# Performance work log

Hardware: AMD Instinct MI355X
Metric: run time of the kernel (lower is better)

Reference implementation:

```python
import jax, jax.numpy as jnp
import numpy as np

B, N, C = 4, 2048, 768
H = 12
D = C // H  # head_dim = 64
SCALE = D ** -0.5


def setup_inputs() -> dict:
    key = jax.random.key(0)
    ks = jax.random.split(key, 9)
    x_q = jax.random.normal(ks[0], (B, N, C), dtype=jnp.float32)
    x_k = jax.random.normal(ks[1], (B, N, C), dtype=jnp.float32)
    x_v = jax.random.normal(ks[2], (B, N, C), dtype=jnp.float32)
    x_u = jax.random.uniform(ks[3], (B, N, C), dtype=jnp.float32)
    s = C ** -0.5
    Wq = jax.random.normal(ks[4], (C, C), dtype=jnp.float32) * s
    Wk = jax.random.normal(ks[5], (C, C), dtype=jnp.float32) * s
    Wv = jax.random.normal(ks[6], (C, C), dtype=jnp.float32) * s
    Wp = jax.random.normal(ks[7], (C, C), dtype=jnp.float32) * s
    bp = jax.random.normal(ks[8], (C,), dtype=jnp.float32) * 0.01
    return {"x_q": x_q, "x_k": x_k, "x_v": x_v, "x_u": x_u,
            "Wq": Wq, "Wk": Wk, "Wv": Wv, "Wp": Wp, "bp": bp}


def reference(x_q, x_k, x_v, x_u, Wq, Wk, Wv, Wp, bp):
    # Linear projections (torch Linear: y = x @ W.T), split into heads [B,H,N,D]
    def to_heads(x, W):
        y = jnp.einsum('bnc,oc->bno', x, W)
        return y.reshape(B, N, H, D).transpose(0, 2, 1, 3)
    q = to_heads(x_q, Wq) * SCALE
    k = to_heads(x_k, Wk)
    v = to_heads(x_v, Wv)
    # Scores [B,H,N,N]
    attn = jnp.einsum('bhqd,bhkd->bhqk', q, k)
    # Uncertainty map: per-query scalar (mean over channels), broadcast over keys & heads
    uc = jnp.mean(x_u, axis=-1)  # [B,N]
    attn = attn * uc[:, None, :, None]
    attn = jax.nn.softmax(attn, axis=-1)
    out = jnp.einsum('bhqk,bhkd->bhqd', attn, v)
    out = out.transpose(0, 2, 1, 3).reshape(B, N, C)
    return jnp.einsum('bnc,oc->bno', out, Wp) + bp
```

## Files before the change

### kernel.cpp

```cpp
#include <hip/hip_runtime.h>
#include <hip/hip_bf16.h>
#include <cstdint>

#define B_ 4
#define N_ 2048
#define C_ 768
#define H_ 12
#define D_ 64
#define QSCALE 0.18033688011112042f

typedef __bf16 bf16x8 __attribute__((ext_vector_type(8)));
typedef float f32x4 __attribute__((ext_vector_type(4)));
typedef float f32x16 __attribute__((ext_vector_type(16)));

__device__ __forceinline__ unsigned f2bs(float x) {
  unsigned u = __builtin_bit_cast(unsigned, x);
  unsigned r = (u + 0x7fffu + ((u >> 16) & 1u)) >> 16;
  return r;
}

__device__ __forceinline__ bf16x8 ldb8(const unsigned short* p) {
  return __builtin_bit_cast(bf16x8, *(const uint4*)p);
}

__device__ __forceinline__ f32x4 mfma16(bf16x8 a, bf16x8 b, f32x4 c) {
  return __builtin_amdgcn_mfma_f32_16x16x32_bf16(a, b, c, 0, 0, 0);
}

__device__ __forceinline__ f32x16 mfma32(bf16x8 a, bf16x8 b, f32x16 c) {
  return __builtin_amdgcn_mfma_f32_32x32x16_bf16(a, b, c, 0, 0, 0);
}

__device__ __forceinline__ void async16(const unsigned short* g, unsigned short* l) {
  __builtin_amdgcn_global_load_lds(
      (const __attribute__((address_space(1))) unsigned int*)g,
      (__attribute__((address_space(3))) unsigned int*)l, 16, 0, 0);
}

__global__ void prep_kernel(
    const float* __restrict__ xq, const float* __restrict__ xk,
    const float* __restrict__ xv, const float* __restrict__ xu,
    const float* __restrict__ Wq, const float* __restrict__ Wk,
    const float* __restrict__ Wv, const float* __restrict__ Wp,
    unsigned short* __restrict__ dxq, unsigned short* __restrict__ dxk,
    unsigned short* __restrict__ dxv,
    unsigned short* __restrict__ dwq, unsigned short* __restrict__ dwk,
    unsigned short* __restrict__ dwv, unsigned short* __restrict__ dwp,
    float* __restrict__ uc) {
  const int id = blockIdx.x;
  if (id < 5184) {
    const float* s;
    unsigned short* d;
    int sub;
    if (id < 4608) {
      s = (id < 1536) ? xq : (id < 3072) ? xk : xv;
      d = (id < 1536) ? dxq : (id < 3072) ? dxk : dxv;
      sub = (id < 1536) ? id : (id < 3072) ? (id - 1536) : (id - 3072);
    } else {
      int t = id - 4608;
      int which = t / 144;
      s = (which == 0) ? Wq : (which == 1) ? Wk : (which == 2) ? Wv : Wp;
      d = (which == 0) ? dwq : (which == 1) ? dwk : (which == 2) ? dwv : dwp;
      sub = t % 144;
    }
    const int base = sub * 4096 + (int)threadIdx.x * 4;
#pragma unroll
    for (int st = 0; st < 4; ++st) {
      int i = base + st * 1024;
      float4 v = *(const float4*)(s + i);
      ushort4 h;
      h.x = (unsigned short)f2bs(v.x); h.y = (unsigned short)f2bs(v.y);
      h.z = (unsigned short)f2bs(v.z); h.w = (unsigned short)f2bs(v.w);
      *(ushort4*)(d + i) = h;
    }
  } else {
    int sub = id - 5184;
    int w = threadIdx.x >> 6, lane = threadIdx.x & 63;
    int row = sub * 4 + w;
    const float* p = xu + (size_t)row * C_;
    float s = 0.f;
#pragma unroll
    for (int i = 0; i < 3; ++i) {
      float4 v = *(const float4*)(p + (i * 64 + lane) * 4);
      s += v.x + v.y + v.z + v.w;
    }
#pragma unroll
    for (int off = 1; off < 64; off <<= 1) s += __shfl_xor(s, off);
    if (lane == 0) uc[row] = s * (1.f / 768.f);
  }
}

#define TSTR 136
__global__ __launch_bounds__(256, 3) void gemm_qkv(
    const unsigned short* __restrict__ xq, const unsigned short* __restrict__ xk,
    const unsigned short* __restrict__ xv,
    const unsigned short* __restrict__ wq, const unsigned short* __restrict__ wk,
    const unsigned short* __restrict__ wv,
    unsigned short* __restrict__ oq, unsigned short* __restrict__ ok,
    unsigned short* __restrict__ ov, const float* __restrict__ uc) {
  __shared__ __align__(16) unsigned short S[192 * TSTR];
  unsigned short* Al = S;
  unsigned short* Bl = S + 8192;
  const int tid = threadIdx.x;
  const int w = tid >> 6, lane = tid & 63, quad = lane >> 4, id15 = lane & 15;
  const int wm = (w >> 1) << 6, wn = (w & 1) * 96;
  const int id = blockIdx.x;
  const int xcd = id & 7, slot = id >> 3;
  const int n0 = (slot & 3) * 192;
  const int gz = xcd * 24 + (slot >> 2);
  const int z = gz >> 6, m0 = (gz & 63) << 7;

  const unsigned short* A = (z == 0) ? xq : (z == 1) ? xk : xv;
  const unsigned short* W = (z == 0) ? wq : (z == 1) ? wk : wv;

  const int wb = tid & 192;
  const unsigned short* ap[4];
#pragma unroll
  for (int s = 0; s < 4; ++s) {
    int g = s * 256 + tid;
    int row = (g >> 2) & 127;
    int col = ((g >> 9) << 5) | ((g & 3) << 3);
    ap[s] = A + (size_t)(m0 + row) * C_ + col;
  }
  const unsigned short* bp[6];
#pragma unroll
  for (int s = 0; s < 6; ++s) {
    int g = s * 256 + tid;
    int r4 = g >> 2;
    int pan = (g >= 768) ? 1 : 0;
    int row = r4 - pan * 192;
    int col = pan * 32 + ((g & 3) << 3);
    bp[s] = W + (size_t)(n0 + row) * C_ + col;
  }

  f32x4 acc[4][6] = {};
  for (int kt = 0; kt < C_; kt += 64) {
    __syncthreads();
#pragma unroll
    for (int s = 0; s < 4; ++s) async16(ap[s] + kt, Al + (s * 256 + wb) * 8);
#pragma unroll
    for (int s = 0; s < 6; ++s) async16(bp[s] + kt, Bl + (s * 256 + wb) * 8);
    __syncthreads();

#pragma unroll
    for (int kk = 0; kk < 2; ++kk) {
      bf16x8 af[4], bfr[6];
#pragma unroll
      for (int i = 0; i < 4; ++i)
        af[i]  = ldb8(&Al[kk * 4096 + (wm + i * 16 + id15) * 32 + quad * 8]);
#pragma unroll
      for (int j = 0; j < 6; ++j)
        bfr[j] = ldb8(&Bl[kk * 6144 + (wn + j * 16 + id15) * 32 + quad * 8]);
#pragma unroll
      for (int i = 0; i < 4; ++i)
#pragma unroll
        for (int j = 0; j < 6; ++j)
          acc[i][j] = mfma16(af[i], bfr[j], acc[i][j]);
    }
  }

  if (z == 2) {
    __syncthreads();
#pragma unroll
    for (int i = 0; i < 4; ++i)
#pragma unroll
      for (int j = 0; j < 6; ++j) {
        uint2 u;
        u.x = f2bs(acc[i][j][0]) | (f2bs(acc[i][j][1]) << 16);
        u.y = f2bs(acc[i][j][2]) | (f2bs(acc[i][j][3]) << 16);
        *(uint2*)&S[(wn + j * 16 + id15) * TSTR + wm + i * 16 + quad * 4] = u;
      }
    __syncthreads();
    const int b = m0 >> 11, nb = m0 & (N_ - 1);
#pragma unroll
    for (int s = 0; s < 12; ++s) {
      int c = s * 256 + tid;
      int row = c >> 4, o = (c & 15) << 3;
      *(uint4*)(ov + (size_t)(b * C_ + n0 + row) * N_ + nb + o) = *(const uint4*)&S[row * TSTR + o];
    }
    return;
  }

#pragma unroll
  for (int i = 0; i < 4; ++i) {
#pragma unroll
    for (int j = 0; j < 6; ++j) {
#pragma unroll
      for (int r = 0; r < 4; ++r) {
        int gm = m0 + wm + i * 16 + quad * 4 + r;
        int gn = n0 + wn + j * 16 + id15;
        float v = acc[i][j][r];
        if (z == 0) {
          v *= QSCALE * uc[gm];
          oq[(size_t)gm * C_ + gn] = (unsigned short)f2bs(v);
        } else {
          ok[(size_t)gm * C_ + gn] = (unsigned short)f2bs(v);
        }
      }
    }
  }
}

__global__ __launch_bounds__(256, 4) void gemm_out(
    const unsigned short* __restrict__ ao, const unsigned short* __restrict__ wp,
    float* __restrict__ out, const float* __restrict__ bias) {
  __shared__ __align__(16) unsigned short Al[64 * 64];
  __shared__ __align__(16) unsigned short Bl[128 * 64];
  const int tid = threadIdx.x;
  const int w = tid >> 6, lane = tid & 63, quad = lane >> 4, id15 = lane & 15;
  const int wm = (w >> 1) << 5, wn = (w & 1) << 6;
  const int id = blockIdx.x;
  const int xcd = id & 7, slot = id >> 3;
  const int n0 = (slot % 6) << 7;
  const int m0 = (xcd * 16 + slot / 6) << 6;

  const int wb = tid & 192;
  const unsigned short* ap[2];
#pragma unroll
  for (int s = 0; s < 2; ++s) {
    int g = s * 256 + tid;
    int row = (g >> 2) & 63;
    int col = ((g >> 8) << 5) | ((g & 3) << 3);
    ap[s] = ao + (size_t)(m0 + row) * C_ + col;
  }
  const unsigned short* bp[4];
#pragma unroll
  for (int s = 0; s < 4; ++s) {
    int g = s * 256 + tid;
    int row = (g >> 2) & 127;
    int col = ((g >> 9) << 5) | ((g & 3) << 3);
    bp[s] = wp + (size_t)(n0 + row) * C_ + col;
  }

  f32x4 acc[2][4] = {};
  for (int kt = 0; kt < C_; kt += 64) {
    __syncthreads();
#pragma unroll
    for (int s = 0; s < 2; ++s) async16(ap[s] + kt, Al + (s * 256 + wb) * 8);
#pragma unroll
    for (int s = 0; s < 4; ++s) async16(bp[s] + kt, Bl + (s * 256 + wb) * 8);
    __syncthreads();

#pragma unroll
    for (int kk = 0; kk < 2; ++kk) {
      bf16x8 af[2], bfr[4];
#pragma unroll
      for (int i = 0; i < 2; ++i)
        af[i]  = ldb8(&Al[kk * 2048 + (wm + i * 16 + id15) * 32 + quad * 8]);
#pragma unroll
      for (int j = 0; j < 4; ++j)
        bfr[j] = ldb8(&Bl[kk * 4096 + (wn + j * 16 + id15) * 32 + quad * 8]);
#pragma unroll
      for (int i = 0; i < 2; ++i)
#pragma unroll
        for (int j = 0; j < 4; ++j)
          acc[i][j] = mfma16(af[i], bfr[j], acc[i][j]);
    }
  }

#pragma unroll
  for (int i = 0; i < 2; ++i) {
#pragma unroll
    for (int j = 0; j < 4; ++j) {
#pragma unroll
      for (int r = 0; r < 4; ++r) {
        int gm = m0 + wm + i * 16 + quad * 4 + r;
        int gn = n0 + wn + j * 16 + id15;
        out[(size_t)gm * C_ + gn] = acc[i][j][r] + bias[gn];
      }
    }
  }
}

#define KSTR 72
#define VOFF (64 * KSTR)
#define BUFO (2 * 64 * KSTR)
__global__ __launch_bounds__(256, 3) void attn_kernel(
    const unsigned short* __restrict__ Q, const unsigned short* __restrict__ Kk,
    const unsigned short* __restrict__ Vt, unsigned short* __restrict__ O) {
  __shared__ __align__(16) unsigned short KV[2 * 2 * 64 * KSTR];

  const int tid = threadIdx.x;
  const int w = tid >> 6, lane = tid & 63;
  const int i32 = lane & 31, hi = lane >> 5;
  const int id = blockIdx.x;
  const int xcd = id & 7, slot = id >> 3;
  const int bh = xcd * 6 + (slot >> 4);
  const int qt = slot & 15;
  const int b = bh / H_, h = bh % H_;
  const int q0 = qt * 128 + w * 32;

  bf16x8 qf[4];
#pragma unroll
  for (int s = 0; s < 4; ++s)
    qf[s] = ldb8(Q + (size_t)(b * N_ + q0 + i32) * C_ + h * 64 + s * 16 + hi * 8);

  const uint4 onesu = {0x3F803F80u, 0x3F803F80u, 0x3F803F80u, 0x3F803F80u};
  const bf16x8 onesf = __builtin_bit_cast(bf16x8, onesu);

  f32x16 oacc0 = {}, oacc1 = {}, lacc = {};

  const size_t kbase = (size_t)(b * N_) * C_ + h * 64;
  const size_t vbase = (size_t)(b * C_ + h * 64) * N_;
  const int srow0 = tid >> 3, srow1 = 32 + (tid >> 3);
  const int sseg = (tid & 7) << 3;

  {
    uint4 a0 = *(const uint4*)(Kk + kbase + (size_t)srow0 * C_ + sseg);
    uint4 a1 = *(const uint4*)(Kk + kbase + (size_t)srow1 * C_ + sseg);
    uint4 c0 = *(const uint4*)(Vt + vbase + (size_t)srow0 * N_ + sseg);
    uint4 c1 = *(const uint4*)(Vt + vbase + (size_t)srow1 * N_ + sseg);
    *(uint4*)&KV[srow0 * KSTR + sseg] = a0;
    *(uint4*)&KV[srow1 * KSTR + sseg] = a1;
    *(uint4*)&KV[VOFF + srow0 * KSTR + sseg] = c0;
    *(uint4*)&KV[VOFF + srow1 * KSTR + sseg] = c1;
  }

  int cur = 0;
  for (int kc = 0; kc < N_; kc += 64) {
    const bool last = (kc + 64 >= N_);
    uint4 a0, a1, c0, c1;
    if (!last) {
      const int kcn = kc + 64;
      a0 = *(const uint4*)(Kk + kbase + (size_t)(kcn + srow0) * C_ + sseg);
      a1 = *(const uint4*)(Kk + kbase + (size_t)(kcn + srow1) * C_ + sseg);
      c0 = *(const uint4*)(Vt + vbase + (size_t)srow0 * N_ + kcn + sseg);
      c1 = *(const uint4*)(Vt + vbase + (size_t)srow1 * N_ + kcn + sseg);
    }

    asm volatile("s_waitcnt lgkmcnt(0)" ::: "memory");
    __builtin_amdgcn_s_barrier();

    const unsigned short* Kc = KV + (cur ? BUFO : 0);
    const unsigned short* Vc = Kc + VOFF;
#pragma unroll
    for (int t = 0; t < 2; ++t) {
      f32x16 s16 = {};
      __builtin_amdgcn_s_setprio(1);
#pragma unroll
      for (int s = 0; s < 4; ++s) {
        bf16x8 kf = ldb8(Kc + (t * 32 + i32) * KSTR + s * 16 + hi * 8);
        s16 = mfma32(kf, qf[s], s16);
      }
      __builtin_amdgcn_s_setprio(0);
      unsigned Dw[8];
#pragma unroll
      for (int j = 0; j < 8; ++j) {
        float e0 = exp2f(s16[2 * j]);
        float e1 = exp2f(s16[2 * j + 1]);
        unsigned d;
        asm("v_cvt_pk_bf16_f32 %0, %1, %2" : "=v"(d) : "v"(e0), "v"(e1));
        Dw[j] = d;
      }
      __builtin_amdgcn_s_setprio(1);
#pragma unroll
      for (int sl = 0; sl < 2; ++sl) {
        const int bb = sl * 4;
        unsigned x0 = Dw[bb + 0], y0 = Dw[bb + 2];
        unsigned x1 = Dw[bb + 1], y1 = Dw[bb + 3];
        asm("v_permlane32_swap_b32 %0, %1" : "+v"(x0), "+v"(y0));
        asm("v_permlane32_swap_b32 %0, %1" : "+v"(x1), "+v"(y1));
        uint4 u;
        u.x = x0;
        u.y = x1;
        u.z = y0;
        u.w = y1;
        bf16x8 pf = __builtin_bit_cast(bf16x8, u);
        lacc = mfma32(pf, onesf, lacc);
        bf16x8 v0 = ldb8(Vc + i32 * KSTR + (2 * t + sl) * 16 + hi * 8);
        bf16x8 v1 = ldb8(Vc + (32 + i32) * KSTR + (2 * t + sl) * 16 + hi * 8);
        oacc0 = mfma32(pf, v0, oacc0);
        oacc1 = mfma32(pf, v1, oacc1);
      }
      __builtin_amdgcn_s_setprio(0);
    }

    if (!last) {
      unsigned short* Kn = KV + (cur ? 0 : BUFO);
      *(uint4*)&Kn[srow0 * KSTR + sseg] = a0;
      *(uint4*)&Kn[srow1 * KSTR + sseg] = a1;
      *(uint4*)&Kn[VOFF + srow0 * KSTR + sseg] = c0;
      *(uint4*)&Kn[VOFF + srow1 * KSTR + sseg] = c1;
    }
    cur ^= 1;
  }

#pragma unroll
  for (int r = 0; r < 16; ++r) {
    float linv = 1.0f / lacc[r];
    int q = q0 + (r & 3) + 8 * (r >> 2) + 4 * hi;
    size_t base = (size_t)(b * N_ + q) * C_ + h * 64 + i32;
    O[base] = (unsigned short)f2bs(oacc0[r] * linv);
    O[base + 32] = (unsigned short)f2bs(oacc1[r] * linv);
  }
}

extern "C" void kernel_launch(void* const* d_in, const int* in_sizes, int n_in,
                              void* d_out, int out_size, void* d_ws, size_t ws_size,
                              hipStream_t stream) {
  const float* x_q = (const float*)d_in[0];
  const float* x_k = (const float*)d_in[1];
  const float* x_v = (const float*)d_in[2];
  const float* x_u = (const float*)d_in[3];
  const float* Wq  = (const float*)d_in[4];
  const float* Wk  = (const float*)d_in[5];
  const float* Wv  = (const float*)d_in[6];
  const float* Wp  = (const float*)d_in[7];
  const float* bp  = (const float*)d_in[8];

  char* ws = (char*)d_ws;
  size_t off = 0;
  auto alloc = [&](size_t bytes) {
    char* p = ws + off;
    off += (bytes + 255) & ~(size_t)255;
    return p;
  };
  unsigned short* wq16 = (unsigned short*)alloc((size_t)C_ * C_ * 2);
  unsigned short* wk16 = (unsigned short*)alloc((size_t)C_ * C_ * 2);
  unsigned short* wv16 = (unsigned short*)alloc((size_t)C_ * C_ * 2);
  unsigned short* wp16 = (unsigned short*)alloc((size_t)C_ * C_ * 2);
  float*          ucp  = (float*)alloc((size_t)B_ * N_ * 4);
  unsigned short* xq16 = (unsigned short*)alloc((size_t)B_ * N_ * C_ * 2);
  unsigned short* xk16 = (unsigned short*)alloc((size_t)B_ * N_ * C_ * 2);
  unsigned short* xv16 = (unsigned short*)alloc((size_t)B_ * N_ * C_ * 2);
  unsigned short* q_s  = (unsigned short*)alloc((size_t)B_ * N_ * C_ * 2);
  unsigned short* k_s  = (unsigned short*)alloc((size_t)B_ * N_ * C_ * 2);
  unsigned short* vT   = (unsigned short*)alloc((size_t)B_ * N_ * C_ * 2);
  unsigned short* ao   = (unsigned short*)alloc((size_t)B_ * N_ * C_ * 2);

  prep_kernel<<<dim3(7232), 256, 0, stream>>>(x_q, x_k, x_v, x_u, Wq, Wk, Wv, Wp,
                                              xq16, xk16, xv16,
                                              wq16, wk16, wv16, wp16, ucp);
  gemm_qkv<<<dim3(768), 256, 0, stream>>>(xq16, xk16, xv16, wq16, wk16, wv16,
                                          q_s, k_s, vT, ucp);
  attn_kernel<<<dim3(768), 256, 0, stream>>>(q_s, k_s, vT, ao);
  gemm_out<<<dim3(768), 256, 0, stream>>>(ao, wp16, (float*)d_out, bp);
}
```

Baseline: 282.8 us.

## Double-buffer LDS K-tiles with async prefetch in QKV and output GEMMs

Both projection GEMMs now step K by 32 instead of 64 and use two LDS buffers. The next tile is prefetched asynchronously while MFMAs run on the current one, with partial vmcnt waits and raw s_barrier replacing the paired __syncthreads. This aims to hide global-load latency behind compute, at the cost of twice as many loop iterations and barriers with less work per step. The QKV kernel reuses its existing shared array, so occupancy stays the same.

```diff
diff --git a/kernel.cpp b/kernel.cpp
--- a/kernel.cpp
+++ b/kernel.cpp
@@ -91,6 +91,7 @@
 }
 
 #define TSTR 136
+#define QBUF 10240
 __global__ __launch_bounds__(256, 3) void gemm_qkv(
     const unsigned short* __restrict__ xq, const unsigned short* __restrict__ xk,
     const unsigned short* __restrict__ xv,
@@ -99,8 +100,6 @@
     unsigned short* __restrict__ oq, unsigned short* __restrict__ ok,
     unsigned short* __restrict__ ov, const float* __restrict__ uc) {
   __shared__ __align__(16) unsigned short S[192 * TSTR];
-  unsigned short* Al = S;
-  unsigned short* Bl = S + 8192;
   const int tid = threadIdx.x;
   const int w = tid >> 6, lane = tid & 63, quad = lane >> 4, id15 = lane & 15;
   const int wm = (w >> 1) << 6, wn = (w & 1) * 96;
@@ -114,49 +113,55 @@
   const unsigned short* W = (z == 0) ? wq : (z == 1) ? wk : wv;
 
   const int wb = tid & 192;
-  const unsigned short* ap[4];
-#pragma unroll
-  for (int s = 0; s < 4; ++s) {
+  const unsigned short* ap[2];
+#pragma unroll
+  for (int s = 0; s < 2; ++s) {
     int g = s * 256 + tid;
-    int row = (g >> 2) & 127;
-    int col = ((g >> 9) << 5) | ((g & 3) << 3);
-    ap[s] = A + (size_t)(m0 + row) * C_ + col;
-  }
-  const unsigned short* bp[6];
-#pragma unroll
-  for (int s = 0; s < 6; ++s) {
+    ap[s] = A + (size_t)(m0 + (g >> 2)) * C_ + ((g & 3) << 3);
+  }
+  const unsigned short* bp[3];
+#pragma unroll
+  for (int s = 0; s < 3; ++s) {
     int g = s * 256 + tid;
-    int r4 = g >> 2;
-    int pan = (g >= 768) ? 1 : 0;
-    int row = r4 - pan * 192;
-    int col = pan * 32 + ((g & 3) << 3);
-    bp[s] = W + (size_t)(n0 + row) * C_ + col;
-  }
+    bp[s] = W + (size_t)(n0 + (g >> 2)) * C_ + ((g & 3) << 3);
+  }
+
+#pragma unroll
+  for (int s = 0; s < 2; ++s) async16(ap[s], S + (s * 256 + wb) * 8);
+#pragma unroll
+  for (int s = 0; s < 3; ++s) async16(bp[s], S + 4096 + (s * 256 + wb) * 8);
 
   f32x4 acc[4][6] = {};
-  for (int kt = 0; kt < C_; kt += 64) {
-    __syncthreads();
-#pragma unroll
-    for (int s = 0; s < 4; ++s) async16(ap[s] + kt, Al + (s * 256 + wb) * 8);
-#pragma unroll
-    for (int s = 0; s < 6; ++s) async16(bp[s] + kt, Bl + (s * 256 + wb) * 8);
-    __syncthreads();
-
-#pragma unroll
-    for (int kk = 0; kk < 2; ++kk) {
-      bf16x8 af[4], bfr[6];
-#pragma unroll
-      for (int i = 0; i < 4; ++i)
-        af[i]  = ldb8(&Al[kk * 4096 + (wm + i * 16 + id15) * 32 + quad * 8]);
+  int cur = 0;
+  for (int kt = 0; kt < C_; kt += 32) {
+    unsigned short* nb = S + (cur ? 0 : QBUF);
+    __builtin_amdgcn_s_barrier();
+    if (kt + 32 < C_) {
+#pragma unroll
+      for (int s = 0; s < 2; ++s) async16(ap[s] + kt + 32, nb + (s * 256 + wb) * 8);
+#pragma unroll
+      for (int s = 0; s < 3; ++s) async16(bp[s] + kt + 32, nb + 4096 + (s * 256 + wb) * 8);
+      asm volatile("s_waitcnt vmcnt(5)" ::: "memory");
+    } else {
+      asm volatile("s_waitcnt vmcnt(0)" ::: "memory");
+    }
+    __builtin_amdgcn_s_barrier();
+
+    const unsigned short* Ab = S + (cur ? QBUF : 0);
+    const unsigned short* Bb = Ab + 4096;
+    bf16x8 af[4], bfr[6];
+#pragma unroll
+    for (int i = 0; i < 4; ++i)
+      af[i]  = ldb8(&Ab[(wm + i * 16 + id15) * 32 + quad * 8]);
+#pragma unroll
+    for (int j = 0; j < 6; ++j)
+      bfr[j] = ldb8(&Bb[(wn + j * 16 + id15) * 32 + quad * 8]);
+#pragma unroll
+    for (int i = 0; i < 4; ++i)
 #pragma unroll
       for (int j = 0; j < 6; ++j)
-        bfr[j] = ldb8(&Bl[kk * 6144 + (wn + j * 16 + id15) * 32 + quad * 8]);
-#pragma unroll
-      for (int i = 0; i < 4; ++i)
-#pragma unroll
-        for (int j = 0; j < 6; ++j)
-          acc[i][j] = mfma16(af[i], bfr[j], acc[i][j]);
-    }
+        acc[i][j] = mfma16(af[i], bfr[j], acc[i][j]);
+    cur ^= 1;
   }
 
   if (z == 2) {
@@ -171,12 +176,12 @@
         *(uint2*)&S[(wn + j * 16 + id15) * TSTR + wm + i * 16 + quad * 4] = u;
       }
     __syncthreads();
-    const int b = m0 >> 11, nb = m0 & (N_ - 1);
+    const int b = m0 >> 11, nb2 = m0 & (N_ - 1);
 #pragma unroll
     for (int s = 0; s < 12; ++s) {
       int c = s * 256 + tid;
       int row = c >> 4, o = (c & 15) << 3;
-      *(uint4*)(ov + (size_t)(b * C_ + n0 + row) * N_ + nb + o) = *(const uint4*)&S[row * TSTR + o];
+      *(uint4*)(ov + (size_t)(b * C_ + n0 + row) * N_ + nb2 + o) = *(const uint4*)&S[row * TSTR + o];
     }
     return;
   }
@@ -201,11 +206,11 @@
   }
 }
 
+#define OBUF 6144
 __global__ __launch_bounds__(256, 4) void gemm_out(
     const unsigned short* __restrict__ ao, const unsigned short* __restrict__ wp,
     float* __restrict__ out, const float* __restrict__ bias) {
-  __shared__ __align__(16) unsigned short Al[64 * 64];
-  __shared__ __align__(16) unsigned short Bl[128 * 64];
+  __shared__ __align__(16) unsigned short S[2 * OBUF];
   const int tid = threadIdx.x;
   const int w = tid >> 6, lane = tid & 63, quad = lane >> 4, id15 = lane & 15;
   const int wm = (w >> 1) << 5, wn = (w & 1) << 6;
@@ -215,47 +220,48 @@
   const int m0 = (xcd * 16 + slot / 6) << 6;
 
   const int wb = tid & 192;
-  const unsigned short* ap[2];
+  const unsigned short* ap0 = ao + (size_t)(m0 + (tid >> 2)) * C_ + ((tid & 3) << 3);
+  const unsigned short* bp[2];
 #pragma unroll
   for (int s = 0; s < 2; ++s) {
     int g = s * 256 + tid;
-    int row = (g >> 2) & 63;
-    int col = ((g >> 8) << 5) | ((g & 3) << 3);
-    ap[s] = ao + (size_t)(m0 + row) * C_ + col;
-  }
-  const unsigned short* bp[4];
-#pragma unroll
-  for (int s = 0; s < 4; ++s) {
-    int g = s * 256 + tid;
-    int row = (g >> 2) & 127;
-    int col = ((g >> 9) << 5) | ((g & 3) << 3);
-    bp[s] = wp + (size_t)(n0 + row) * C_ + col;
-  }
+    bp[s] = wp + (size_t)(n0 + (g >> 2)) * C_ + ((g & 3) << 3);
+  }
+
+  async16(ap0, S + wb * 8);
+#pragma unroll
+  for (int s = 0; s < 2; ++s) async16(bp[s], S + 2048 + (s * 256 + wb) * 8);
 
   f32x4 acc[2][4] = {};
-  for (int kt = 0; kt < C_; kt += 64) {
-    __syncthreads();
-#pragma unroll
-    for (int s = 0; s < 2; ++s) async16(ap[s] + kt, Al + (s * 256 + wb) * 8);
-#pragma unroll
-    for (int s = 0; s < 4; ++s) async16(bp[s] + kt, Bl + (s * 256 + wb) * 8);
-    __syncthreads();
-
-#pragma unroll
-    for (int kk = 0; kk < 2; ++kk) {
-      bf16x8 af[2], bfr[4];
-#pragma unroll
-      for (int i = 0; i < 2; ++i)
-        af[i]  = ldb8(&Al[kk * 2048 + (wm + i * 16 + id15) * 32 + quad * 8]);
+  int cur = 0;
+  for (int kt = 0; kt < C_; kt += 32) {
+    unsigned short* nb = S + (cur ? 0 : OBUF);
+    __builtin_amdgcn_s_barrier();
+    if (kt + 32 < C_) {
+      async16(ap0 + kt + 32, nb + wb * 8);
+#pragma unroll
+      for (int s = 0; s < 2; ++s) async16(bp[s] + kt + 32, nb + 2048 + (s * 256 + wb) * 8);
+      asm volatile("s_waitcnt vmcnt(3)" ::: "memory");
+    } else {
+      asm volatile("s_waitcnt vmcnt(0)" ::: "memory");
+    }
+    __builtin_amdgcn_s_barrier();
+
+    const unsigned short* Ab = S + (cur ? OBUF : 0);
+    const unsigned short* Bb = Ab + 2048;
+    bf16x8 af[2], bfr[4];
+#pragma unroll
+    for (int i = 0; i < 2; ++i)
+      af[i]  = ldb8(&Ab[(wm + i * 16 + id15) * 32 + quad * 8]);
+#pragma unroll
+    for (int j = 0; j < 4; ++j)
+      bfr[j] = ldb8(&Bb[(wn + j * 16 + id15) * 32 + quad * 8]);
+#pragma unroll
+    for (int i = 0; i < 2; ++i)
 #pragma unroll
       for (int j = 0; j < 4; ++j)
-        bfr[j] = ldb8(&Bl[kk * 4096 + (wn + j * 16 + id15) * 32 + quad * 8]);
-#pragma unroll
-      for (int i = 0; i < 2; ++i)
-#pragma unroll
-        for (int j = 0; j < 4; ++j)
-          acc[i][j] = mfma16(af[i], bfr[j], acc[i][j]);
-    }
+        acc[i][j] = mfma16(af[i], bfr[j], acc[i][j]);
+    cur ^= 1;
   }
 
 #pragma unroll
```

New measurement: 290.1 us. +2.6%, slower.

## Fuse fp32-to-bf16 activation conversion into QKV GEMM A-tile loads

Applied to the files above, without the earlier changes.

The separate prep pass that converted x_q/x_k/x_v to bf16 in global memory is removed. The QKV GEMM now reads fp32 activations directly, packs them with v_cvt_pk_bf16_f32 and stores them to LDS, while weights still arrive via async global-to-LDS loads. This drops a full write and re-read of three bf16 activation tensors. In exchange the A-tile load becomes synchronous through registers, and each activation tile is fetched at twice the bytes once per N-tile block, since 4 column blocks re-read the same rows.

```diff
diff --git a/kernel.cpp b/kernel.cpp
--- a/kernel.cpp
+++ b/kernel.cpp
@@ -37,32 +37,25 @@
       (__attribute__((address_space(3))) unsigned int*)l, 16, 0, 0);
 }
 
+__device__ __forceinline__ unsigned pkbf(float lo, float hi) {
+  unsigned d;
+  asm("v_cvt_pk_bf16_f32 %0, %1, %2" : "=v"(d) : "v"(lo), "v"(hi));
+  return d;
+}
+
 __global__ void prep_kernel(
-    const float* __restrict__ xq, const float* __restrict__ xk,
-    const float* __restrict__ xv, const float* __restrict__ xu,
+    const float* __restrict__ xu,
     const float* __restrict__ Wq, const float* __restrict__ Wk,
     const float* __restrict__ Wv, const float* __restrict__ Wp,
-    unsigned short* __restrict__ dxq, unsigned short* __restrict__ dxk,
-    unsigned short* __restrict__ dxv,
     unsigned short* __restrict__ dwq, unsigned short* __restrict__ dwk,
     unsigned short* __restrict__ dwv, unsigned short* __restrict__ dwp,
     float* __restrict__ uc) {
   const int id = blockIdx.x;
-  if (id < 5184) {
-    const float* s;
-    unsigned short* d;
-    int sub;
-    if (id < 4608) {
-      s = (id < 1536) ? xq : (id < 3072) ? xk : xv;
-      d = (id < 1536) ? dxq : (id < 3072) ? dxk : dxv;
-      sub = (id < 1536) ? id : (id < 3072) ? (id - 1536) : (id - 3072);
-    } else {
-      int t = id - 4608;
-      int which = t / 144;
-      s = (which == 0) ? Wq : (which == 1) ? Wk : (which == 2) ? Wv : Wp;
-      d = (which == 0) ? dwq : (which == 1) ? dwk : (which == 2) ? dwv : dwp;
-      sub = t % 144;
-    }
+  if (id < 576) {
+    int which = id / 144;
+    const float* s = (which == 0) ? Wq : (which == 1) ? Wk : (which == 2) ? Wv : Wp;
+    unsigned short* d = (which == 0) ? dwq : (which == 1) ? dwk : (which == 2) ? dwv : dwp;
+    int sub = id - which * 144;
     const int base = sub * 4096 + (int)threadIdx.x * 4;
 #pragma unroll
     for (int st = 0; st < 4; ++st) {
@@ -74,7 +67,7 @@
       *(ushort4*)(d + i) = h;
     }
   } else {
-    int sub = id - 5184;
+    int sub = id - 576;
     int w = threadIdx.x >> 6, lane = threadIdx.x & 63;
     int row = sub * 4 + w;
     const float* p = xu + (size_t)row * C_;
@@ -92,8 +85,8 @@
 
 #define TSTR 136
 __global__ __launch_bounds__(256, 3) void gemm_qkv(
-    const unsigned short* __restrict__ xq, const unsigned short* __restrict__ xk,
-    const unsigned short* __restrict__ xv,
+    const float* __restrict__ xqf, const float* __restrict__ xkf,
+    const float* __restrict__ xvf,
     const unsigned short* __restrict__ wq, const unsigned short* __restrict__ wk,
     const unsigned short* __restrict__ wv,
     unsigned short* __restrict__ oq, unsigned short* __restrict__ ok,
@@ -110,17 +103,19 @@
   const int gz = xcd * 24 + (slot >> 2);
   const int z = gz >> 6, m0 = (gz & 63) << 7;
 
-  const unsigned short* A = (z == 0) ? xq : (z == 1) ? xk : xv;
+  const float* A32 = (z == 0) ? xqf : (z == 1) ? xkf : xvf;
   const unsigned short* W = (z == 0) ? wq : (z == 1) ? wk : wv;
 
   const int wb = tid & 192;
-  const unsigned short* ap[4];
+  const float* ap[4];
+  int adst[4];
 #pragma unroll
   for (int s = 0; s < 4; ++s) {
     int g = s * 256 + tid;
     int row = (g >> 2) & 127;
     int col = ((g >> 9) << 5) | ((g & 3) << 3);
-    ap[s] = A + (size_t)(m0 + row) * C_ + col;
+    ap[s] = A32 + (size_t)(m0 + row) * C_ + col;
+    adst[s] = g * 8;
   }
   const unsigned short* bp[6];
 #pragma unroll
@@ -137,9 +132,18 @@
   for (int kt = 0; kt < C_; kt += 64) {
     __syncthreads();
 #pragma unroll
-    for (int s = 0; s < 4; ++s) async16(ap[s] + kt, Al + (s * 256 + wb) * 8);
-#pragma unroll
     for (int s = 0; s < 6; ++s) async16(bp[s] + kt, Bl + (s * 256 + wb) * 8);
+#pragma unroll
+    for (int s = 0; s < 4; ++s) {
+      float4 u0 = *(const float4*)(ap[s] + kt);
+      float4 u1 = *(const float4*)(ap[s] + kt + 4);
+      uint4 pk;
+      pk.x = pkbf(u0.x, u0.y);
+      pk.y = pkbf(u0.z, u0.w);
+      pk.z = pkbf(u1.x, u1.y);
+      pk.w = pkbf(u1.z, u1.w);
+      *(uint4*)&Al[adst[s]] = pk;
+    }
     __syncthreads();
 
 #pragma unroll
@@ -171,12 +175,12 @@
         *(uint2*)&S[(wn + j * 16 + id15) * TSTR + wm + i * 16 + quad * 4] = u;
       }
     __syncthreads();
-    const int b = m0 >> 11, nb = m0 & (N_ - 1);
+    const int b = m0 >> 11, nb2 = m0 & (N_ - 1);
 #pragma unroll
     for (int s = 0; s < 12; ++s) {
       int c = s * 256 + tid;
       int row = c >> 4, o = (c & 15) << 3;
-      *(uint4*)(ov + (size_t)(b * C_ + n0 + row) * N_ + nb + o) = *(const uint4*)&S[row * TSTR + o];
+      *(uint4*)(ov + (size_t)(b * C_ + n0 + row) * N_ + nb2 + o) = *(const uint4*)&S[row * TSTR + o];
     }
     return;
   }
@@ -420,18 +424,14 @@
   unsigned short* wv16 = (unsigned short*)alloc((size_t)C_ * C_ * 2);
   unsigned short* wp16 = (unsigned short*)alloc((size_t)C_ * C_ * 2);
   float*          ucp  = (float*)alloc((size_t)B_ * N_ * 4);
-  unsigned short* xq16 = (unsigned short*)alloc((size_t)B_ * N_ * C_ * 2);
-  unsigned short* xk16 = (unsigned short*)alloc((size_t)B_ * N_ * C_ * 2);
-  unsigned short* xv16 = (unsigned short*)alloc((size_t)B_ * N_ * C_ * 2);
   unsigned short* q_s  = (unsigned short*)alloc((size_t)B_ * N_ * C_ * 2);
   unsigned short* k_s  = (unsigned short*)alloc((size_t)B_ * N_ * C_ * 2);
   unsigned short* vT   = (unsigned short*)alloc((size_t)B_ * N_ * C_ * 2);
   unsigned short* ao   = (unsigned short*)alloc((size_t)B_ * N_ * C_ * 2);
 
-  prep_kernel<<<dim3(7232), 256, 0, stream>>>(x_q, x_k, x_v, x_u, Wq, Wk, Wv, Wp,
-                                              xq16, xk16, xv16,
+  prep_kernel<<<dim3(2624), 256, 0, stream>>>(x_u, Wq, Wk, Wv, Wp,
                                               wq16, wk16, wv16, wp16, ucp);
-  gemm_qkv<<<dim3(768), 256, 0, stream>>>(xq16, xk16, xv16, wq16, wk16, wv16,
+  gemm_qkv<<<dim3(768), 256, 0, stream>>>(x_q, x_k, x_v, wq16, wk16, wv16,
                                           q_s, k_s, vT, ucp);
   attn_kernel<<<dim3(768), 256, 0, stream>>>(q_s, k_s, vT, ao);
   gemm_out<<<dim3(768), 256, 0, stream>>>(ao, wp16, (float*)d_out, bp);
```

After: 296.2 us. 4.8% more time.
